# Kernel tuning notes

Measured on AMD Instinct MI355X. Metric: run time of the kernel, lower is better.

The kernel has to match this reference:

```python
import jax, jax.numpy as jnp
import numpy as np

B, T, D, H = 64, 512, 512, 128

def swish(x):
    return x * jax.nn.sigmoid(x)

def setup_inputs() -> dict:
    key = jax.random.key(0)
    ks = jax.random.split(key, 8)
    X = jax.random.normal(ks[0], (B, T, D), dtype=jnp.float32)
    # strictly-upper-triangular random binary adjacency -> valid DAG
    adj = jax.random.bernoulli(ks[1], 0.3, (T, T)).astype(jnp.float32)
    dag = jnp.triu(adj, k=1)
    s = 1.0 / np.sqrt(D)
    Wk = jax.random.normal(ks[2], (H, D), dtype=jnp.float32) * s
    bk = jax.random.normal(ks[3], (H,), dtype=jnp.float32) * 0.01
    Wq = jax.random.normal(ks[4], (H, D), dtype=jnp.float32) * s
    bq = jax.random.normal(ks[5], (H,), dtype=jnp.float32) * 0.01
    Wv = jax.random.normal(ks[6], (H, D), dtype=jnp.float32) * s
    bv = jax.random.normal(ks[7], (H,), dtype=jnp.float32) * 0.01
    return {"X": X, "dag": dag, "Wk": Wk, "bk": bk, "Wq": Wq, "bq": bq, "Wv": Wv, "bv": bv}

def reference(X, dag, Wk, bk, Wq, bq, Wv, bv):
    K = swish(jnp.einsum('btd,hd->bth', X, Wk) + bk)  # [B,T,H]
    Q = swish(jnp.einsum('btd,hd->bth', X, Wq) + bq)
    V = swish(jnp.einsum('btd,hd->bth', X, Wv) + bv)
    S_qk = jnp.einsum('bqh,bkh->bqk', Q, K) / jnp.sqrt(jnp.float32(H))  # [B,T,T]
    dagT = dag.T  # [T,T]
    Sprime = dagT * jnp.einsum('ij,bjk->bik', dagT, S_qk)  # [B,T,T]
    # masked_fill(Sprime == 0, -inf) then softmax; rows that are all -inf
    # would produce NaN in torch and are replaced by zeros -> do it nan-free.
    nz = Sprime != 0
    masked = jnp.where(nz, Sprime, -jnp.inf)
    row_valid = jnp.any(nz, axis=-1, keepdims=True)  # [B,T,1]
    masked_safe = jnp.where(row_valid, masked, 0.0)
    probs = jax.nn.softmax(masked_safe, axis=-1) * row_valid  # [B,T,T]
    Vprime = jnp.einsum('ij,bjh->bih', dagT, V)  # [B,T,H]
    O = jnp.einsum('bqk,bkh->bqh', probs, V) + Vprime
    return O
```

## Files before the change

### kernel.cpp

```cpp
#include <hip/hip_runtime.h>
#include <hip/hip_bf16.h>

#define Bn 64
#define Tn 512
#define Dn 512
#define Hn 128
#define BT (Bn*Tn)

typedef unsigned short u16;
typedef unsigned long long u64;
typedef __attribute__((ext_vector_type(8))) short bf16x8;
typedef __attribute__((ext_vector_type(4))) float f32x4;

__device__ __forceinline__ u16 f2bf(float f) {
  union { float f; unsigned u; } v; v.f = f;
  unsigned r = (v.u + 0x7FFFu + ((v.u >> 16) & 1u)) >> 16;
  return (u16)r;
}

__device__ __forceinline__ bf16x8 pack8(float4 a, float4 b) {
  bf16x8 o;
  o[0] = (short)f2bf(a.x); o[1] = (short)f2bf(a.y);
  o[2] = (short)f2bf(a.z); o[3] = (short)f2bf(a.w);
  o[4] = (short)f2bf(b.x); o[5] = (short)f2bf(b.y);
  o[6] = (short)f2bf(b.z); o[7] = (short)f2bf(b.w);
  return o;
}

__device__ __forceinline__ void gload16(const void* g, void* lds) {
  __builtin_amdgcn_global_load_lds(
      (const __attribute__((address_space(1))) unsigned int*)g,
      (__attribute__((address_space(3))) unsigned int*)lds, 16, 0, 0);
}

__global__ __launch_bounds__(256) void prep(
    const float4* __restrict__ Wk, const float4* __restrict__ Wq,
    const float4* __restrict__ Wv, ushort4* __restrict__ Wcat,
    const float* __restrict__ dag, u16* __restrict__ dagT,
    u64* __restrict__ bits) {
  __shared__ float s[64][65];
  if (blockIdx.x < 192) {
    int idx = blockIdx.x * 256 + threadIdx.x;
    int which = idx >> 14, j = idx & 16383;
    const float4* src = (which == 0) ? Wk : (which == 1) ? Wq : Wv;
    float4 v = src[j];
    ushort4 o; o.x = f2bf(v.x); o.y = f2bf(v.y); o.z = f2bf(v.z); o.w = f2bf(v.w);
    Wcat[idx] = o;
  } else {
    int bid = blockIdx.x - 192;
    int bx = bid & 7, by = bid >> 3;
    int r0 = by * 64, c0 = bx * 64;
    int t = threadIdx.x;
    int c4 = t & 15, rr = t >> 4;
#pragma unroll
    for (int q = 0; q < 4; ++q) {
      int r = rr + q * 16;
      float4 v = *(const float4*)&dag[(size_t)(r0 + r) * Tn + c0 + c4 * 4];
      s[c4 * 4 + 0][r] = v.x; s[c4 * 4 + 1][r] = v.y;
      s[c4 * 4 + 2][r] = v.z; s[c4 * 4 + 3][r] = v.w;
    }
    __syncthreads();
#pragma unroll
    for (int q = 0; q < 4; ++q) {
      int il = rr + q * 16;
      ushort4 o;
      u64 b4 = 0;
#pragma unroll
      for (int r = 0; r < 4; ++r) {
        float v = s[il][c4 * 4 + r];
        ((u16*)&o)[r] = f2bf(v);
        b4 |= (u64)(v != 0.f) << (c4 * 4 + r);
      }
      *(ushort4*)&dagT[(size_t)(c0 + il) * Tn + r0 + c4 * 4] = o;
      b4 |= __shfl_xor(b4, 1, 64);
      b4 |= __shfl_xor(b4, 2, 64);
      b4 |= __shfl_xor(b4, 4, 64);
      b4 |= __shfl_xor(b4, 8, 64);
      if (c4 == 0) bits[(size_t)(c0 + il) * 8 + (r0 >> 6)] = b4;
    }
  }
}

__global__ __launch_bounds__(512, 4) void qkv3(
    const float* __restrict__ X, const u16* __restrict__ Wcat,
    const float* __restrict__ bk, const float* __restrict__ bq,
    const float* __restrict__ bv,
    u16* __restrict__ Kb, u16* __restrict__ QT, u16* __restrict__ VT) {
  __shared__ u16 sm[28672];
  int bid = blockIdx.x;
  int xcd = bid & 7, idx = bid >> 3;
  int b = (idx & 7) * 8 + xcd;
  int rowblk = idx >> 3;
  int m0 = b * Tn + rowblk * 64;
  int tid = threadIdx.x, lane = tid & 63, wave = tid >> 6;
  int col0 = lane & 15, rg = lane >> 4, kcb = rg * 16;
  int swl = (col0 & 7) << 4;
  int xrow = tid >> 3, xc8 = tid & 7;
  f32x4 acc[3][4] = {};
  const char* Wb = (const char*)Wcat;
  char* smb = (char*)sm;

#define LOAD_X(kt_)                                                             \
  {                                                                             \
    const float4* s_ = (const float4*)(X + (size_t)(m0 + xrow) * Dn + (kt_) + xc8 * 8); \
    xa0 = s_[0]; xa1 = s_[1];                                                   \
  }

  float4 xa0, xa1;
  LOAD_X(0);
  for (int kt = 0; kt < Dn; kt += 64) {
    {
      int sw = (xrow & 7) << 4;
      *(bf16x8*)(smb + xrow * 128 + ((xc8 * 16) ^ sw)) = pack8(xa0, xa1);
    }
    if (kt + 64 < Dn) LOAD_X(kt + 64);
#pragma unroll
    for (int q = 0; q < 6; ++q) {
      int c2 = wave * 6 + q;
      int which = c2 >> 4, widx = c2 & 15;
      int flat = widx * 1024 + lane * 16;
      int row = flat >> 7, colb = flat & 127;
      int sw = (row & 7) << 4;
      gload16(Wb + (size_t)which * 131072 + (size_t)row * 1024 + (kt << 1) + (colb ^ sw),
              smb + 8192 + which * 16384 + widx * 1024);
    }
    __syncthreads();
    bf16x8 af[4][2];
#pragma unroll
    for (int m = 0; m < 4; ++m)
#pragma unroll
      for (int kk = 0; kk < 2; ++kk)
        af[m][kk] = *(const bf16x8*)(smb + (m * 16 + col0) * 128 + ((kk * 64 + kcb) ^ swl));
#pragma unroll
    for (int which = 0; which < 3; ++which) {
      bf16x8 bfr[2];
#pragma unroll
      for (int kk = 0; kk < 2; ++kk)
        bfr[kk] = *(const bf16x8*)(smb + 8192 + which * 16384 +
                                   (wave * 16 + col0) * 128 + ((kk * 64 + kcb) ^ swl));
#pragma unroll
      for (int kk = 0; kk < 2; ++kk)
#pragma unroll
        for (int m = 0; m < 4; ++m)
          acc[which][m] = __builtin_amdgcn_mfma_f32_16x16x32_bf16(
              af[m][kk], bfr[kk], acc[which][m], 0, 0, 0);
    }
    __syncthreads();
  }
#undef LOAD_X

  {
    int nl = wave * 16 + col0;
    float bsk = bk[nl], bsq = bq[nl], bsv = bv[nl];
#pragma unroll
    for (int m = 0; m < 4; ++m)
#pragma unroll
      for (int r = 0; r < 4; ++r) {
        int tl = m * 16 + rg * 4 + r;
        float xk = acc[0][m][r] + bsk;
        float xq = acc[1][m][r] + bsq;
        float xv = acc[2][m][r] + bsv;
        *(u16*)(smb + tl * 256 + ((nl * 2) ^ ((tl & 7) << 4))) = f2bf(xk / (1.f + __expf(-xk)));
        *(u16*)(smb + 16384 + nl * 128 + ((tl * 2) ^ ((nl & 7) << 4))) = f2bf(xq / (1.f + __expf(-xq)));
        *(u16*)(smb + 32768 + nl * 128 + ((tl * 2) ^ ((nl & 7) << 4))) = f2bf(xv / (1.f + __expf(-xv)));
      }
    __syncthreads();
    int tt0 = rowblk * 64;
#pragma unroll
    for (int p = 0; p < 2; ++p) {
      int c = p * 512 + tid;
      int t = c >> 4, c16 = c & 15;
      *(bf16x8*)&Kb[(size_t)(m0 + t) * Hn + c16 * 8] =
          *(const bf16x8*)(smb + t * 256 + ((c16 * 16) ^ ((t & 7) << 4)));
    }
#pragma unroll
    for (int p = 0; p < 2; ++p) {
      int c = p * 512 + tid;
      int h = c >> 3, c8 = c & 7;
      *(bf16x8*)&QT[((size_t)b * Hn + h) * Tn + tt0 + c8 * 8] =
          *(const bf16x8*)(smb + 16384 + h * 128 + ((c8 * 16) ^ ((h & 7) << 4)));
      *(bf16x8*)&VT[((size_t)b * Hn + h) * Tn + tt0 + c8 * 8] =
          *(const bf16x8*)(smb + 32768 + h * 128 + ((c8 * 16) ^ ((h & 7) << 4)));
    }
  }
}

__global__ __launch_bounds__(512, 4) void dattn(
    const u16* __restrict__ dagT, const u16* __restrict__ QT,
    const u16* __restrict__ VT, const u16* __restrict__ Kb,
    const u64* __restrict__ dbits, float* __restrict__ O) {
  __shared__ char smA[65536];
  __shared__ u16 smQ2[8192];

  int bid = blockIdx.x;
  int xcd = bid & 7, rst = bid >> 3;
  int bx = rst & 7, b = (rst >> 3) * 8 + xcd;
  int m0 = bx * 64;
  int tid = threadIdx.x, lane = tid & 63, wave = tid >> 6;
  int col0 = lane & 15, g = lane >> 4;
  int swl = (col0 & 7) << 4;
  int grp = wave >> 2, gw = wave & 3;

  const char* Ab = (const char*)(dagT + (size_t)m0 * Tn);
  const char* Qb = (const char*)(QT + (size_t)b * Hn * Tn);
  const char* Vb = (const char*)(VT + (size_t)b * Hn * Tn);
  const char* Kb0 = (const char*)(Kb + (size_t)b * Tn * Hn);

  f32x4 accq[4] = {};
  for (int kt = 0; kt < Tn; kt += 64) {
    {
      int ch = wave;
      int flat = ch * 1024 + lane * 16;
      int row = flat >> 7, colb = flat & 127;
      int sw = (row & 7) << 4;
      gload16(Ab + (size_t)row * 1024 + kt * 2 + (colb ^ sw), smA + ch * 1024);
    }
#pragma unroll
    for (int q = 0; q < 2; ++q) {
      int ch = wave * 2 + q;
      int flat = ch * 1024 + lane * 16;
      int row = flat >> 7, colb = flat & 127;
      int sw = (row & 7) << 4;
      gload16(Qb + (size_t)row * 1024 + kt * 2 + (colb ^ sw), smA + 8192 + ch * 1024);
    }
    __syncthreads();
    bf16x8 af[4][2], fq[2];
#pragma unroll
    for (int m = 0; m < 4; ++m)
#pragma unroll
      for (int kk = 0; kk < 2; ++kk)
        af[m][kk] = *(const bf16x8*)(smA + (m * 16 + col0) * 128 + ((kk * 64 + g * 16) ^ swl));
#pragma unroll
    for (int kk = 0; kk < 2; ++kk)
      fq[kk] = *(const bf16x8*)(smA + 8192 + (wave * 16 + col0) * 128 + ((kk * 64 + g * 16) ^ swl));
#pragma unroll
    for (int kk = 0; kk < 2; ++kk)
#pragma unroll
      for (int m = 0; m < 4; ++m)
        accq[m] = __builtin_amdgcn_mfma_f32_16x16x32_bf16(af[m][kk], fq[kk], accq[m], 0, 0, 0);
    __syncthreads();
  }

  const float scale = 0.08838834764831845f;
#pragma unroll
  for (int m = 0; m < 4; ++m)
#pragma unroll
    for (int r = 0; r < 4; ++r) {
      int q = m * 16 + g * 4 + r;
      int h = wave * 16 + col0;
      *(u16*)((char*)smQ2 + q * 256 + ((h * 2) ^ ((q & 7) << 4))) = f2bf(accq[m][r] * scale);
    }

#define STAGE_K(c_)                                                            \
  {                                                                            \
    _Pragma("unroll")                                                          \
    for (int q = 0; q < 4; ++q) {                                              \
      int ch = gw * 4 + q;                                                     \
      int flat = ch * 1024 + lane * 16;                                        \
      int row = flat >> 8, colb = flat & 255;                                  \
      gload16(Kb0 + (size_t)(grp * 256 + (c_) * 64 + row) * 256 + (colb ^ ((row & 7) << 4)), \
              smA + grp * 32768 + ((c_) & 1) * 16384 + ch * 1024);             \
    }                                                                          \
  }

  STAGE_K(0);
  __syncthreads();

  int qrow = gw * 16 + col0;
  bf16x8 bq[4];
#pragma unroll
  for (int kk = 0; kk < 4; ++kk)
    bq[kk] = *(const bf16x8*)((char*)smQ2 + qrow * 256 + ((kk * 64 + g * 16) ^ ((qrow & 7) << 4)));
  const u64* dbq = dbits + (size_t)(m0 + qrow) * 8;
  u64 md[4];
#pragma unroll
  for (int w = 0; w < 4; ++w) md[w] = dbq[grp * 4 + w];

  f32x4 sa[16] = {};
#pragma unroll
  for (int c = 0; c < 4; ++c) {
    if (c < 3) STAGE_K(c + 1);
    const char* kb = smA + grp * 32768 + (c & 1) * 16384;
#pragma unroll
    for (int t = 0; t < 4; ++t)
#pragma unroll
      for (int kk = 0; kk < 4; ++kk) {
        bf16x8 ak = *(const bf16x8*)(kb + (t * 16 + col0) * 256 + ((kk * 64 + g * 16) ^ swl));
        sa[c * 4 + t] = __builtin_amdgcn_mfma_f32_16x16x32_bf16(ak, bq[kk], sa[c * 4 + t], 0, 0, 0);
      }
    if (c < 3) __syncthreads();
  }

  float mx = -INFINITY;
#pragma unroll
  for (int c = 0; c < 4; ++c)
#pragma unroll
    for (int t = 0; t < 4; ++t)
#pragma unroll
      for (int r = 0; r < 4; ++r) {
        int bit = t * 16 + g * 4 + r;
        float v = ((md[c] >> bit) & 1) ? sa[c * 4 + t][r] : -INFINITY;
        sa[c * 4 + t][r] = v;
        mx = fmaxf(mx, v);
      }
  mx = fmaxf(mx, __shfl_xor(mx, 16, 64));
  mx = fmaxf(mx, __shfl_xor(mx, 32, 64));

  float* redf = (float*)smQ2;
  __syncthreads();
  if (g == 0) redf[qrow * 2 + grp] = mx;
  __syncthreads();
  float mboth = fmaxf(redf[qrow * 2], redf[qrow * 2 + 1]);
  float mm = (mboth == -INFINITY) ? 0.f : mboth;

  float s = 0.f;
#pragma unroll
  for (int i = 0; i < 16; ++i)
#pragma unroll
    for (int r = 0; r < 4; ++r) {
      float v = sa[i][r];
      float e = (v == -INFINITY) ? 0.f : __expf(v - mm);
      sa[i][r] = e;
      s += e;
    }
  s += __shfl_xor(s, 16, 64);
  s += __shfl_xor(s, 32, 64);
  if (g == 0) redf[128 + qrow * 2 + grp] = s;
  __syncthreads();
  float stot = redf[128 + qrow * 2] + redf[128 + qrow * 2 + 1];
  float inv = (stot > 0.f) ? (1.f / stot) : 0.f;

  ushort4 pk[16];
#pragma unroll
  for (int c = 0; c < 4; ++c)
#pragma unroll
    for (int t = 0; t < 4; ++t) {
      ushort4 p;
#pragma unroll
      for (int r = 0; r < 4; ++r) {
        int bit = t * 16 + g * 4 + r;
        float d = (float)((md[c] >> bit) & 1);
        ((u16*)&p)[r] = f2bf(sa[c * 4 + t][r] * inv + d);
      }
      pk[c * 4 + t] = p;
    }

  f32x4 acco[4] = {};
  int sww = (qrow & 7) << 4;

#define WRITE_P(c_, base_)                                                     \
  if (grp == ((c_) >> 1)) {                                                    \
    int cc = (c_) & 1;                                                         \
    _Pragma("unroll")                                                          \
    for (int u = 0; u < 2; ++u)                                                \
      _Pragma("unroll")                                                        \
      for (int t2 = 0; t2 < 4; ++t2)                                           \
        *(ushort4*)((base_) + qrow * 256 + ((u * 128 + t2 * 32 + g * 8) ^ sww)) = \
            pk[(cc * 2 + u) * 4 + t2];                                         \
  }

  __syncthreads();
  WRITE_P(0, smA);
  __syncthreads();
#pragma unroll
  for (int c = 0; c < 4; ++c) {
    const char* pb = smA + (c & 1) * 16384;
    if (c < 3) WRITE_P(c + 1, smA + ((c + 1) & 1) * 16384);
#pragma unroll
    for (int kk = 0; kk < 4; ++kk) {
      bf16x8 pa[4], vb;
#pragma unroll
      for (int m = 0; m < 4; ++m) {
        int row = m * 16 + col0;
        pa[m] = *(const bf16x8*)(pb + row * 256 + ((kk * 64 + g * 16) ^ ((row & 7) << 4)));
      }
      vb = *(const bf16x8*)(Vb + (size_t)(wave * 16 + col0) * 1024 + c * 256 + kk * 64 + g * 16);
#pragma unroll
      for (int m = 0; m < 4; ++m)
        acco[m] = __builtin_amdgcn_mfma_f32_16x16x32_bf16(pa[m], vb, acco[m], 0, 0, 0);
    }
    __syncthreads();
  }

#pragma unroll
  for (int m = 0; m < 4; ++m)
#pragma unroll
    for (int r = 0; r < 4; ++r) {
      int i = m0 + m * 16 + g * 4 + r;
      int h = wave * 16 + col0;
      O[((size_t)b * Tn + i) * Hn + h] = acco[m][r];
    }
#undef STAGE_K
#undef WRITE_P
}

extern "C" void kernel_launch(void* const* d_in, const int* in_sizes, int n_in,
                              void* d_out, int out_size, void* d_ws, size_t ws_size,
                              hipStream_t stream) {
  const float* X   = (const float*)d_in[0];
  const float* dag = (const float*)d_in[1];
  const float* Wk  = (const float*)d_in[2];
  const float* bk  = (const float*)d_in[3];
  const float* Wq  = (const float*)d_in[4];
  const float* bq  = (const float*)d_in[5];
  const float* Wv  = (const float*)d_in[6];
  const float* bv  = (const float*)d_in[7];
  float* O = (float*)d_out;

  char* ws = (char*)d_ws;
  u16* Wcat = (u16*)(ws);
  u16* dagT = (u16*)(ws + 393216);
  u64* dbits= (u64*)(ws + 917504);
  u16* Kb   = (u16*)(ws + 950272);
  u16* QT   = (u16*)(ws + 9338880);
  u16* VT   = (u16*)(ws + 17727488);

  prep<<<256, 256, 0, stream>>>((const float4*)Wk, (const float4*)Wq,
                                (const float4*)Wv, (ushort4*)Wcat, dag, dagT, dbits);
  qkv3<<<BT / 64, 512, 0, stream>>>(X, Wcat, bk, bq, bv, Kb, QT, VT);
  dattn<<<512, 512, 0, stream>>>(dagT, QT, VT, Kb, dbits, O);
}
```

Before: 64.43 us.

## Double-buffer QKV projection with 256-thread blocks and 32-wide K steps

Reworks the QKV projection kernel to use 256 threads per block, each wave computing 32 output columns instead of 16. The K loop now steps by 32 and ping-pongs between two shared-memory buffers, so the next X tile and weight tile are staged while MFMAs run on the current one, and one barrier per iteration is removed. The XOR swizzle on the shared-memory tiles is dropped, which may add LDS bank conflicts, and halving the thread count lowers latency hiding per block.

```diff
diff --git a/kernel.cpp b/kernel.cpp
--- a/kernel.cpp
+++ b/kernel.cpp
@@ -81,7 +81,7 @@
   }
 }
 
-__global__ __launch_bounds__(512, 4) void qkv3(
+__global__ __launch_bounds__(256, 2) void qkv3(
     const float* __restrict__ X, const u16* __restrict__ Wcat,
     const float* __restrict__ bk, const float* __restrict__ bq,
     const float* __restrict__ bv,
@@ -93,89 +93,104 @@
   int rowblk = idx >> 3;
   int m0 = b * Tn + rowblk * 64;
   int tid = threadIdx.x, lane = tid & 63, wave = tid >> 6;
-  int col0 = lane & 15, rg = lane >> 4, kcb = rg * 16;
-  int swl = (col0 & 7) << 4;
-  int xrow = tid >> 3, xc8 = tid & 7;
-  f32x4 acc[3][4] = {};
+  int col0 = lane & 15, rg = lane >> 4;
+  int xrow = tid >> 2, xc8 = tid & 3;
+  f32x4 acc[3][4][2] = {};
   const char* Wb = (const char*)Wcat;
   char* smb = (char*)sm;
+  const int BUF = 28672 / 2;
+
+#define BUFB(p_) ((p_) * 28672)
 
 #define LOAD_X(kt_)                                                             \
   {                                                                             \
     const float4* s_ = (const float4*)(X + (size_t)(m0 + xrow) * Dn + (kt_) + xc8 * 8); \
     xa0 = s_[0]; xa1 = s_[1];                                                   \
   }
+#define PACK_X(p_)                                                              \
+  *(bf16x8*)(smb + BUFB(p_) + xrow * 64 + xc8 * 16) = pack8(xa0, xa1);
+#define STAGE_W(kt_, p_)                                                        \
+  {                                                                             \
+    _Pragma("unroll")                                                           \
+    for (int q = 0; q < 6; ++q) {                                               \
+      int c2 = wave * 6 + q;                           \
+      int which = c2 >> 3, widx = c2 & 7;                                       \
+      int flat = widx * 1024 + lane * 16;                                       \
+      int row = flat >> 6, colb = flat & 63;                                    \
+      gload16(Wb + (size_t)which * 131072 + (size_t)row * 1024 + ((kt_) << 1) + colb, \
+              smb + BUFB(p_) + 4096 + which * 8192 + widx * 1024);              \
+    }                                                                           \
+  }
 
   float4 xa0, xa1;
   LOAD_X(0);
-  for (int kt = 0; kt < Dn; kt += 64) {
-    {
-      int sw = (xrow & 7) << 4;
-      *(bf16x8*)(smb + xrow * 128 + ((xc8 * 16) ^ sw)) = pack8(xa0, xa1);
-    }
-    if (kt + 64 < Dn) LOAD_X(kt + 64);
-#pragma unroll
-    for (int q = 0; q < 6; ++q) {
-      int c2 = wave * 6 + q;
-      int which = c2 >> 4, widx = c2 & 15;
-      int flat = widx * 1024 + lane * 16;
-      int row = flat >> 7, colb = flat & 127;
-      int sw = (row & 7) << 4;
-      gload16(Wb + (size_t)which * 131072 + (size_t)row * 1024 + (kt << 1) + (colb ^ sw),
-              smb + 8192 + which * 16384 + widx * 1024);
-    }
-    __syncthreads();
-    bf16x8 af[4][2];
+  PACK_X(0);
+  LOAD_X(32);
+  STAGE_W(0, 0);
+  __syncthreads();
+
+  for (int kt = 0; kt < Dn; kt += 32) {
+    int p = (kt >> 5) & 1;
+    if (kt + 32 < Dn) {
+      PACK_X(p ^ 1);
+      if (kt + 64 < Dn) LOAD_X(kt + 64);
+      STAGE_W(kt + 32, p ^ 1);
+    }
+    bf16x8 af[4];
 #pragma unroll
     for (int m = 0; m < 4; ++m)
-#pragma unroll
-      for (int kk = 0; kk < 2; ++kk)
-        af[m][kk] = *(const bf16x8*)(smb + (m * 16 + col0) * 128 + ((kk * 64 + kcb) ^ swl));
+      af[m] = *(const bf16x8*)(smb + BUFB(p) + (m * 16 + col0) * 64 + rg * 16);
 #pragma unroll
     for (int which = 0; which < 3; ++which) {
       bf16x8 bfr[2];
 #pragma unroll
-      for (int kk = 0; kk < 2; ++kk)
-        bfr[kk] = *(const bf16x8*)(smb + 8192 + which * 16384 +
-                                   (wave * 16 + col0) * 128 + ((kk * 64 + kcb) ^ swl));
-#pragma unroll
-      for (int kk = 0; kk < 2; ++kk)
-#pragma unroll
-        for (int m = 0; m < 4; ++m)
-          acc[which][m] = __builtin_amdgcn_mfma_f32_16x16x32_bf16(
-              af[m][kk], bfr[kk], acc[which][m], 0, 0, 0);
+      for (int n = 0; n < 2; ++n)
+        bfr[n] = *(const bf16x8*)(smb + BUFB(p) + 4096 + which * 8192 +
+                                  (wave * 32 + n * 16 + col0) * 64 + rg * 16);
+#pragma unroll
+      for (int m = 0; m < 4; ++m)
+#pragma unroll
+        for (int n = 0; n < 2; ++n)
+          acc[which][m][n] = __builtin_amdgcn_mfma_f32_16x16x32_bf16(
+              af[m], bfr[n], acc[which][m][n], 0, 0, 0);
     }
     __syncthreads();
   }
 #undef LOAD_X
+#undef PACK_X
+#undef STAGE_W
+#undef BUFB
 
   {
-    int nl = wave * 16 + col0;
-    float bsk = bk[nl], bsq = bq[nl], bsv = bv[nl];
-#pragma unroll
-    for (int m = 0; m < 4; ++m)
-#pragma unroll
-      for (int r = 0; r < 4; ++r) {
-        int tl = m * 16 + rg * 4 + r;
-        float xk = acc[0][m][r] + bsk;
-        float xq = acc[1][m][r] + bsq;
-        float xv = acc[2][m][r] + bsv;
-        *(u16*)(smb + tl * 256 + ((nl * 2) ^ ((tl & 7) << 4))) = f2bf(xk / (1.f + __expf(-xk)));
-        *(u16*)(smb + 16384 + nl * 128 + ((tl * 2) ^ ((nl & 7) << 4))) = f2bf(xq / (1.f + __expf(-xq)));
-        *(u16*)(smb + 32768 + nl * 128 + ((tl * 2) ^ ((nl & 7) << 4))) = f2bf(xv / (1.f + __expf(-xv)));
-      }
+#pragma unroll
+    for (int n = 0; n < 2; ++n) {
+      int nl = wave * 32 + n * 16 + col0;
+      float bsk = bk[nl], bsq = bq[nl], bsv = bv[nl];
+#pragma unroll
+      for (int m = 0; m < 4; ++m)
+#pragma unroll
+        for (int r = 0; r < 4; ++r) {
+          int tl = m * 16 + rg * 4 + r;
+          float xk = acc[0][m][n][r] + bsk;
+          float xq = acc[1][m][n][r] + bsq;
+          float xv = acc[2][m][n][r] + bsv;
+          *(u16*)(smb + tl * 256 + ((nl * 2) ^ ((tl & 7) << 4))) = f2bf(xk / (1.f + __expf(-xk)));
+          *(u16*)(smb + 16384 + nl * 128 + ((tl * 2) ^ ((nl & 7) << 4))) = f2bf(xq / (1.f + __expf(-xq)));
+          *(u16*)(smb + 32768 + nl * 128 + ((tl * 2) ^ ((nl & 7) << 4))) = f2bf(xv / (1.f + __expf(-xv)));
+        }
+    }
     __syncthreads();
     int tt0 = rowblk * 64;
 #pragma unroll
-    for (int p = 0; p < 2; ++p) {
-      int c = p * 512 + tid;
+    for (int p = 0; p < 4; ++p) {
+      int c = p * 256 + tid;
       int t = c >> 4, c16 = c & 15;
       *(bf16x8*)&Kb[(size_t)(m0 + t) * Hn + c16 * 8] =
           *(const bf16x8*)(smb + t * 256 + ((c16 * 16) ^ ((t & 7) << 4)));
     }
 #pragma unroll
-    for (int p = 0; p < 2; ++p) {
-      int c = p * 512 + tid;
+    for (int p = 0; p < 4; ++p) {
+      int c = p * 256 + tid;
       int h = c >> 3, c8 = c & 7;
       *(bf16x8*)&QT[((size_t)b * Hn + h) * Tn + tt0 + c8 * 8] =
           *(const bf16x8*)(smb + 16384 + h * 128 + ((c8 * 16) ^ ((h & 7) << 4)));
@@ -417,6 +432,6 @@
 
   prep<<<256, 256, 0, stream>>>((const float4*)Wk, (const float4*)Wq,
                                 (const float4*)Wv, (ushort4*)Wcat, dag, dagT, dbits);
-  qkv3<<<BT / 64, 512, 0, stream>>>(X, Wcat, bk, bq, bv, Kb, QT, VT);
+  qkv3<<<BT / 64, 256, 0, stream>>>(X, Wcat, bk, bq, bv, Kb, QT, VT);
   dattn<<<512, 512, 0, stream>>>(dagT, QT, VT, Kb, dbits, O);
 }
```

Measured after the change: 67.92 us. 1.05x slower.

## Halve qkv3 block to 256 threads with two N-tiles per wave; use intrinsic bf16 convert

Applied to the files above, without the earlier changes.

The QKV projection kernel now runs 4 waves per block instead of 8. Each wave computes two 16-column tiles per matrix, which doubles the accumulators and gives more MFMA work per A-fragment LDS load. Each thread now loads 16 floats of X and issues 12 weight global-to-LDS loads per k-step. The hand-written round-to-nearest bf16 conversion is replaced by __float2bfloat16. This cuts fragment reloads and barrier participants but raises register pressure and lowers occupancy per block.

```diff
diff --git a/kernel.cpp b/kernel.cpp
--- a/kernel.cpp
+++ b/kernel.cpp
@@ -13,9 +13,9 @@
 typedef __attribute__((ext_vector_type(4))) float f32x4;
 
 __device__ __forceinline__ u16 f2bf(float f) {
-  union { float f; unsigned u; } v; v.f = f;
-  unsigned r = (v.u + 0x7FFFu + ((v.u >> 16) & 1u)) >> 16;
-  return (u16)r;
+  union { __hip_bfloat16 h; u16 u; } v;
+  v.h = __float2bfloat16(f);
+  return v.u;
 }
 
 __device__ __forceinline__ bf16x8 pack8(float4 a, float4 b) {
@@ -81,7 +81,7 @@
   }
 }
 
-__global__ __launch_bounds__(512, 4) void qkv3(
+__global__ __launch_bounds__(256, 2) void qkv3(
     const float* __restrict__ X, const u16* __restrict__ Wcat,
     const float* __restrict__ bk, const float* __restrict__ bq,
     const float* __restrict__ bv,
@@ -95,28 +95,29 @@
   int tid = threadIdx.x, lane = tid & 63, wave = tid >> 6;
   int col0 = lane & 15, rg = lane >> 4, kcb = rg * 16;
   int swl = (col0 & 7) << 4;
-  int xrow = tid >> 3, xc8 = tid & 7;
-  f32x4 acc[3][4] = {};
+  int xrow = tid >> 2, xcq = tid & 3;
+  f32x4 acc[3][4][2] = {};
   const char* Wb = (const char*)Wcat;
   char* smb = (char*)sm;
 
 #define LOAD_X(kt_)                                                             \
   {                                                                             \
-    const float4* s_ = (const float4*)(X + (size_t)(m0 + xrow) * Dn + (kt_) + xc8 * 8); \
-    xa0 = s_[0]; xa1 = s_[1];                                                   \
-  }
-
-  float4 xa0, xa1;
+    const float4* s_ = (const float4*)(X + (size_t)(m0 + xrow) * Dn + (kt_) + xcq * 16); \
+    xa0 = s_[0]; xa1 = s_[1]; xa2 = s_[2]; xa3 = s_[3];                         \
+  }
+
+  float4 xa0, xa1, xa2, xa3;
   LOAD_X(0);
   for (int kt = 0; kt < Dn; kt += 64) {
     {
       int sw = (xrow & 7) << 4;
-      *(bf16x8*)(smb + xrow * 128 + ((xc8 * 16) ^ sw)) = pack8(xa0, xa1);
+      *(bf16x8*)(smb + xrow * 128 + ((xcq * 32) ^ sw)) = pack8(xa0, xa1);
+      *(bf16x8*)(smb + xrow * 128 + ((xcq * 32 + 16) ^ sw)) = pack8(xa2, xa3);
     }
     if (kt + 64 < Dn) LOAD_X(kt + 64);
 #pragma unroll
-    for (int q = 0; q < 6; ++q) {
-      int c2 = wave * 6 + q;
+    for (int q = 0; q < 12; ++q) {
+      int c2 = wave * 12 + q;
       int which = c2 >> 4, widx = c2 & 15;
       int flat = widx * 1024 + lane * 16;
       int row = flat >> 7, colb = flat & 127;
@@ -133,49 +134,56 @@
         af[m][kk] = *(const bf16x8*)(smb + (m * 16 + col0) * 128 + ((kk * 64 + kcb) ^ swl));
 #pragma unroll
     for (int which = 0; which < 3; ++which) {
-      bf16x8 bfr[2];
+      bf16x8 bfr[2][2];
+#pragma unroll
+      for (int n = 0; n < 2; ++n)
+#pragma unroll
+        for (int kk = 0; kk < 2; ++kk)
+          bfr[n][kk] = *(const bf16x8*)(smb + 8192 + which * 16384 +
+                                        (wave * 32 + n * 16 + col0) * 128 + ((kk * 64 + kcb) ^ swl));
 #pragma unroll
       for (int kk = 0; kk < 2; ++kk)
-        bfr[kk] = *(const bf16x8*)(smb + 8192 + which * 16384 +
-                                   (wave * 16 + col0) * 128 + ((kk * 64 + kcb) ^ swl));
-#pragma unroll
-      for (int kk = 0; kk < 2; ++kk)
 #pragma unroll
         for (int m = 0; m < 4; ++m)
-          acc[which][m] = __builtin_amdgcn_mfma_f32_16x16x32_bf16(
-              af[m][kk], bfr[kk], acc[which][m], 0, 0, 0);
+#pragma unroll
+          for (int n = 0; n < 2; ++n)
+            acc[which][m][n] = __builtin_amdgcn_mfma_f32_16x16x32_bf16(
+                af[m][kk], bfr[n][kk], acc[which][m][n], 0, 0, 0);
     }
     __syncthreads();
   }
 #undef LOAD_X
 
   {
-    int nl = wave * 16 + col0;
-    float bsk = bk[nl], bsq = bq[nl], bsv = bv[nl];
-#pragma unroll
-    for (int m = 0; m < 4; ++m)
-#pragma unroll
-      for (int r = 0; r < 4; ++r) {
-        int tl = m * 16 + rg * 4 + r;
-        float xk = acc[0][m][r] + bsk;
-        float xq = acc[1][m][r] + bsq;
-        float xv = acc[2][m][r] + bsv;
-        *(u16*)(smb + tl * 256 + ((nl * 2) ^ ((tl & 7) << 4))) = f2bf(xk / (1.f + __expf(-xk)));
-        *(u16*)(smb + 16384 + nl * 128 + ((tl * 2) ^ ((nl & 7) << 4))) = f2bf(xq / (1.f + __expf(-xq)));
-        *(u16*)(smb + 32768 + nl * 128 + ((tl * 2) ^ ((nl & 7) << 4))) = f2bf(xv / (1.f + __expf(-xv)));
-      }
+#pragma unroll
+    for (int n = 0; n < 2; ++n) {
+      int nl = wave * 32 + n * 16 + col0;
+      float bsk = bk[nl], bsq = bq[nl], bsv = bv[nl];
+#pragma unroll
+      for (int m = 0; m < 4; ++m)
+#pragma unroll
+        for (int r = 0; r < 4; ++r) {
+          int tl = m * 16 + rg * 4 + r;
+          float xk = acc[0][m][n][r] + bsk;
+          float xq = acc[1][m][n][r] + bsq;
+          float xv = acc[2][m][n][r] + bsv;
+          *(u16*)(smb + tl * 256 + ((nl * 2) ^ ((tl & 7) << 4))) = f2bf(xk / (1.f + __expf(-xk)));
+          *(u16*)(smb + 16384 + nl * 128 + ((tl * 2) ^ ((nl & 7) << 4))) = f2bf(xq / (1.f + __expf(-xq)));
+          *(u16*)(smb + 32768 + nl * 128 + ((tl * 2) ^ ((nl & 7) << 4))) = f2bf(xv / (1.f + __expf(-xv)));
+        }
+    }
     __syncthreads();
     int tt0 = rowblk * 64;
 #pragma unroll
-    for (int p = 0; p < 2; ++p) {
-      int c = p * 512 + tid;
+    for (int p = 0; p < 4; ++p) {
+      int c = p * 256 + tid;
       int t = c >> 4, c16 = c & 15;
       *(bf16x8*)&Kb[(size_t)(m0 + t) * Hn + c16 * 8] =
           *(const bf16x8*)(smb + t * 256 + ((c16 * 16) ^ ((t & 7) << 4)));
     }
 #pragma unroll
-    for (int p = 0; p < 2; ++p) {
-      int c = p * 512 + tid;
+    for (int p = 0; p < 4; ++p) {
+      int c = p * 256 + tid;
       int h = c >> 3, c8 = c & 7;
       *(bf16x8*)&QT[((size_t)b * Hn + h) * Tn + tt0 + c8 * 8] =
           *(const bf16x8*)(smb + 16384 + h * 128 + ((c8 * 16) ^ ((h & 7) << 4)));
@@ -417,6 +425,6 @@
 
   prep<<<256, 256, 0, stream>>>((const float4*)Wk, (const float4*)Wq,
                                 (const float4*)Wv, (ushort4*)Wcat, dag, dagT, dbits);
-  qkv3<<<BT / 64, 512, 0, stream>>>(X, Wcat, bk, bq, bv, Kb, QT, VT);
+  qkv3<<<BT / 64, 256, 0, stream>>>(X, Wcat, bk, bq, bv, Kb, QT, VT);
   dattn<<<512, 512, 0, stream>>>(dagT, QT, VT, Kb, dbits, O);
 }
```

After: 65.63 us. Within noise of the previous version (+1.9%).
